# Optimization experiments

Measured on AMD Instinct MI355X. Metric: run time of the kernel, lower is better.

The kernel has to match this reference:

```python
import jax, jax.numpy as jnp
import numpy as np

NEIGHBOR_N = 3  # hard-coded in the torch module
EPS = 1e-6


def setup_inputs() -> dict:
    key = jax.random.key(0)
    k1, k2 = jax.random.split(key)
    B, P, D = 2048, 100000, 128
    sess_emb = jax.random.normal(k1, (B, D), dtype=jnp.float32)
    pool_emb = jax.random.normal(k2, (P, D), dtype=jnp.float32)
    return {"sess_emb": sess_emb, "pool_emb": pool_emb}


def reference(sess_emb, pool_emb):
    # cosine similarity: [B, P]
    fenzi = jnp.matmul(sess_emb, pool_emb.T)
    fenmu_l = jnp.sqrt(jnp.sum(sess_emb * sess_emb + EPS, axis=1))[:, None]   # [B,1]
    fenmu_r = jnp.sqrt(jnp.sum(pool_emb * pool_emb + EPS, axis=1))[None, :]   # [1,P]
    cos_sim = jax.nn.softmax(fenzi / (fenmu_l * fenmu_r), axis=-1)            # [B,P]

    k_v = min(NEIGHBOR_N, cos_sim.shape[0])
    cos_topk, topk_indice = jax.lax.top_k(cos_sim, k_v)                       # [B,k], [B,k]
    cos_topk = jax.nn.softmax(cos_topk, axis=-1)

    sess_topk = pool_emb[topk_indice]                                         # [B,k,D] gather
    neighbor_sess = jnp.sum(cos_topk[..., None] * sess_topk, axis=1)          # [B,D]
    # dropout40 is identity in eval mode; reference is deterministic
    return (neighbor_sess, cos_topk, sess_topk)
```

## Files before the change

kernel.cpp:

```cpp
#include <hip/hip_runtime.h>
#include <math.h>

#define B_ROWS 2048
#define P_ROWS 100000
#define D_DIM  128
#define NPC    64
#define NT     782
#define TILEB  32768
#define NCAND  (NPC * 3)

typedef short short8 __attribute__((ext_vector_type(8)));
typedef float f32x4  __attribute__((ext_vector_type(4)));
typedef unsigned long long u64;

__device__ __forceinline__ unsigned short f2bf(float f) {
    unsigned u = __float_as_uint(f);
    u += 0x7fffu + ((u >> 16) & 1u);
    return (unsigned short)(u >> 16);
}

__device__ __forceinline__ void async16(const char* g, char* l) {
    __builtin_amdgcn_global_load_lds(
        (const __attribute__((address_space(1))) unsigned int*)g,
        (__attribute__((address_space(3))) unsigned int*)l,
        16, 0, 0);
}

__device__ __forceinline__ void kins64(u64 k, u64& t0, u64& t1, u64& t2) {
    u64 m0 = (t0 < k) ? t0 : k;  t0 = (t0 < k) ? k : t0;
    u64 m1 = (t1 < m0) ? t1 : m0; t1 = (t1 < m0) ? m0 : t1;
    t2 = (t2 < m1) ? m1 : t2;
}

__device__ __forceinline__ void ins3d(double v, int c,
                                      double& v0, int& i0,
                                      double& v1, int& i1,
                                      double& v2, int& i2) {
    bool b0 = (v > v0) || (v == v0 && c < i0);
    bool b1 = (v > v1) || (v == v1 && c < i1);
    bool b2 = (v > v2) || (v == v2 && c < i2);
    if (b0)      { v2 = v1; i2 = i1; v1 = v0; i1 = i0; v0 = v; i0 = c; }
    else if (b1) { v2 = v1; i2 = i1; v1 = v;  i1 = c; }
    else if (b2) { v2 = v;  i2 = c; }
}

__global__ void pack_sess_kernel(const float* __restrict__ sess,
                                 char* __restrict__ sess2) {
    int row  = blockIdx.x * 4 + (threadIdx.x >> 6);
    int lane = threadIdx.x & 63;
    float2 v = ((const float2*)(sess + (size_t)row * D_DIM))[lane];
    float s = v.x * v.x + v.y * v.y;
    #pragma unroll
    for (int o = 32; o > 0; o >>= 1) s += __shfl_xor(s, o);
    float inv = 1.0f / sqrtf(s + (float)D_DIM * 1e-6f);
    ushort2 hv;
    hv.x = f2bf(v.x * inv);
    hv.y = f2bf(v.y * inv);
    *(ushort2*)(sess2 + (size_t)row * 256 + lane * 4) = hv;
}

__global__ void pack_pool_kernel(const float* __restrict__ pool,
                                 char* __restrict__ pool2,
                                 float* __restrict__ S_part) {
    __shared__ float red[128][17];
    __shared__ float s_inv[128];
    __shared__ float red2[16][128];
    const int tid = threadIdx.x;
    const int T   = blockIdx.x;
    const int c0  = tid >> 4;
    const int g   = tid & 15;

    #pragma unroll
    for (int it = 0; it < 8; ++it) {
        int c = it * 16 + c0;
        int n = T * 128 + c;
        float4 a = make_float4(0.f, 0.f, 0.f, 0.f), b = a;
        if (n < P_ROWS) {
            const float4* src = (const float4*)(pool + (size_t)n * D_DIM + g * 8);
            a = src[0]; b = src[1];
        }
        red[c][g] = a.x*a.x + a.y*a.y + a.z*a.z + a.w*a.w
                  + b.x*b.x + b.y*b.y + b.z*b.z + b.w*b.w;
    }
    __syncthreads();
    if (tid < 128) {
        float s = 0.f;
        #pragma unroll
        for (int j = 0; j < 16; ++j) s += red[tid][j];
        s_inv[tid] = 1.0f / sqrtf(s + (float)D_DIM * 1e-6f);
    }
    __syncthreads();

    float sacc[8] = {0.f,0.f,0.f,0.f,0.f,0.f,0.f,0.f};
    #pragma unroll
    for (int it = 0; it < 8; ++it) {
        int c = it * 16 + c0;
        int n = T * 128 + c;
        float4 a = make_float4(0.f, 0.f, 0.f, 0.f), b = a;
        if (n < P_ROWS) {
            const float4* src = (const float4*)(pool + (size_t)n * D_DIM + g * 8);
            a = src[0]; b = src[1];
        }
        float inv = s_inv[c];
        const float f[8] = {a.x, a.y, a.z, a.w, b.x, b.y, b.z, b.w};
        short8 hv;
        #pragma unroll
        for (int j = 0; j < 8; ++j) {
            float w = f[j] * inv;
            hv[j] = (short)f2bf(w);
            sacc[j] += w;
        }
        *(short8*)(pool2 + (size_t)T * TILEB + c * 256 + ((g ^ (c & 7)) * 16)) = hv;
    }
    #pragma unroll
    for (int j = 0; j < 8; ++j) red2[c0][g * 8 + j] = sacc[j];
    __syncthreads();
    if (tid < 128) {
        float s = 0.f;
        #pragma unroll
        for (int k = 0; k < 16; ++k) s += red2[k][tid];
        S_part[(size_t)T * 128 + tid] = s;
    }
}

__global__ void reduce_S_kernel(const float* __restrict__ S_part,
                                float* __restrict__ S) {
    __shared__ float part[256];
    const int d = blockIdx.x;
    float s = 0.f;
    for (int T = threadIdx.x; T < NT; T += 256)
        s += S_part[(size_t)T * 128 + d];
    part[threadIdx.x] = s;
    __syncthreads();
    #pragma unroll
    for (int o = 128; o > 0; o >>= 1) {
        if (threadIdx.x < o) part[threadIdx.x] += part[threadIdx.x + o];
        __syncthreads();
    }
    if (threadIdx.x == 0) S[d] = part[0];
}

__launch_bounds__(256, 2)
__global__ void gemm_topk_kernel(const char* __restrict__ sess2,
                                 const char* __restrict__ pool2,
                                 u64* __restrict__ partials) {
    __shared__ char lds[TILEB];

    const int tid = threadIdx.x;
    const int w   = tid >> 6;
    const int L   = tid & 63;
    const int q   = L >> 4;
    const int l15 = L & 15;
    const int l7  = L & 7;
    const int pc  = blockIdx.x;
    const int mt  = blockIdx.y;
    const int rowbase = mt * 128 + w * 32;

    short8 afrag[2][4];
    #pragma unroll
    for (int i = 0; i < 2; ++i)
        #pragma unroll
        for (int ks = 0; ks < 4; ++ks)
            afrag[i][ks] = *(const short8*)(sess2 +
                (size_t)(rowbase + i * 16 + l15) * 256 + (ks * 4 + q) * 16);

    int soks[4];
    #pragma unroll
    for (int ks = 0; ks < 4; ++ks) soks[ks] = ((ks * 4 + q) ^ l7) * 16;
    const char* lbase = lds + l15 * 256;

    float key0[2][4], key1[2][4], key2[2][4];
    #pragma unroll
    for (int i = 0; i < 2; ++i)
        #pragma unroll
        for (int r = 0; r < 4; ++r)
            key0[i][r] = key1[i][r] = key2[i][r] = -1e30f;

    int tloc = 0;
    for (int T = pc; T < NT; T += NPC, ++tloc) {
        __syncthreads();
        const char* tb = pool2 + (size_t)T * TILEB;
        #pragma unroll
        for (int rr = 0; rr < 8; ++rr) {
            int idx = rr * 256 + tid;
            async16(tb + idx * 16, lds + idx * 16);
        }
        __syncthreads();

        #pragma unroll
        for (int qt = 0; qt < 4; ++qt) {
            f32x4 acc[2][2];
            #pragma unroll
            for (int i = 0; i < 2; ++i) {
                acc[i][0] = (f32x4){0.f,0.f,0.f,0.f};
                acc[i][1] = (f32x4){0.f,0.f,0.f,0.f};
            }
            #pragma unroll
            for (int ks = 0; ks < 4; ++ks) {
                const char* cb = lbase + qt * 8192 + soks[ks];
                short8 b0 = *(const short8*)(cb);
                short8 b1 = *(const short8*)(cb + 16 * 256);
                #pragma unroll
                for (int i = 0; i < 2; ++i) {
                    acc[i][0] = __builtin_amdgcn_mfma_f32_16x16x32_bf16(
                        afrag[i][ks], b0, acc[i][0], 0, 0, 0);
                    acc[i][1] = __builtin_amdgcn_mfma_f32_16x16x32_bf16(
                        afrag[i][ks], b1, acc[i][1], 0, 0, 0);
                }
            }
            #pragma unroll
            for (int j = 0; j < 2; ++j) {
                const unsigned pos = (unsigned)(tloc * 8 + qt * 2 + j);
                #pragma unroll
                for (int i = 0; i < 2; ++i)
                    #pragma unroll
                    for (int r = 0; r < 4; ++r) {
                        float v = acc[i][j][r];
                        float kf = __uint_as_float(
                            (__float_as_uint(v) & 0xFFFFFF80u) | pos);
                        float o0 = key0[i][r], o1 = key1[i][r];
                        key0[i][r] = fmaxf(o0, kf);
                        key1[i][r] = __builtin_amdgcn_fmed3f(kf, o0, key1[i][r]);
                        key2[i][r] = __builtin_amdgcn_fmed3f(kf, o1, key2[i][r]);
                    }
            }
        }
    }

    #pragma unroll
    for (int i = 0; i < 2; ++i)
        #pragma unroll
        for (int r = 0; r < 4; ++r) {
            float kk[3] = {key0[i][r], key1[i][r], key2[i][r]};
            u64 t0 = 0ull, t1 = 0ull, t2 = 0ull;
            #pragma unroll
            for (int k = 0; k < 3; ++k) {
                unsigned u   = __float_as_uint(kk[k]);
                unsigned pos = u & 127u;
                unsigned vb  = u & 0xFFFFFF80u;
                unsigned mono = (vb & 0x80000000u) ? ~vb : (vb | 0x80000000u);
                unsigned col = (unsigned)((pc + (int)(pos >> 3) * NPC) * 128
                                          + (int)(pos & 7u) * 16 + l15);
                u64 key = ((u64)mono << 32) | (u64)(131071u - col);
                kins64(key, t0, t1, t2);
            }
            #pragma unroll
            for (int m = 1; m < 16; m <<= 1) {
                u64 r0 = __shfl_xor(t0, m);
                u64 r1 = __shfl_xor(t1, m);
                u64 r2 = __shfl_xor(t2, m);
                kins64(r0, t0, t1, t2);
                kins64(r1, t0, t1, t2);
                kins64(r2, t0, t1, t2);
            }
            if (l15 == 0) {
                int row = rowbase + i * 16 + q * 4 + r;
                u64* o = partials + ((size_t)row * NPC + pc) * 3;
                o[0] = t0; o[1] = t1; o[2] = t2;
            }
        }
}

__launch_bounds__(256)
__global__ void finalize_kernel(const float* __restrict__ sess,
                                const float* __restrict__ pool,
                                const u64* __restrict__ partials,
                                const float* __restrict__ S,
                                float* __restrict__ out_neighbor,
                                float* __restrict__ out_costopk,
                                float* __restrict__ out_sesstopk) {
    __shared__ u64    keys[NCAND];
    __shared__ u64    top8[8];
    __shared__ double vv[8];
    __shared__ int    ii[8];
    __shared__ double s_na, s_dss;
    __shared__ float  s_w[3];
    __shared__ int    s_i[3];

    const int row = blockIdx.x;
    const int tid = threadIdx.x;
    const int w   = tid >> 6;
    const int L   = tid & 63;

    if (tid < NCAND) keys[tid] = partials[(size_t)row * NCAND + tid];
    if (w == 3) {
        float2 sa = ((const float2*)(sess + (size_t)row * D_DIM))[L];
        double na  = (double)sa.x * sa.x + (double)sa.y * sa.y;
        double dss = (double)sa.x * S[2 * L] + (double)sa.y * S[2 * L + 1];
        #pragma unroll
        for (int o = 32; o > 0; o >>= 1) {
            na  += __shfl_xor(na, o);
            dss += __shfl_xor(dss, o);
        }
        if (L == 0) { s_na = na + (double)D_DIM * 1e-6; s_dss = dss; }
    }
    __syncthreads();

    if (w == 0) {
        for (int k = 0; k < 8; ++k) {
            u64 a0 = keys[L], a1 = keys[L + 64], a2 = keys[L + 128];
            u64 m = a0 > a1 ? a0 : a1;
            m = m > a2 ? m : a2;
            u64 g = m;
            #pragma unroll
            for (int o = 1; o < 64; o <<= 1) {
                u64 r = __shfl_xor(g, o);
                g = (r > g) ? r : g;
            }
            if (m == g && g != 0ull) {
                if (a0 == g)      keys[L] = 0ull;
                else if (a1 == g) keys[L + 64] = 0ull;
                else              keys[L + 128] = 0ull;
            }
            if (L == 0) top8[k] = g;
        }
    }
    __syncthreads();

    {
        float2 sa = ((const float2*)(sess + (size_t)row * D_DIM))[L];
        for (int cc = 0; cc < 2; ++cc) {
            int c = 2 * w + cc;
            int idx = 131071 - (int)(top8[c] & 0x1FFFFull);
            bool ok = idx < P_ROWS;
            float2 pb = ok ? ((const float2*)(pool + (size_t)idx * D_DIM))[L]
                           : make_float2(0.f, 0.f);
            double dot = (double)sa.x * pb.x + (double)sa.y * pb.y;
            double nb  = (double)pb.x * pb.x + (double)pb.y * pb.y;
            #pragma unroll
            for (int o = 32; o > 0; o >>= 1) {
                dot += __shfl_xor(dot, o);
                nb  += __shfl_xor(nb, o);
            }
            if (L == 0) {
                vv[c] = ok ? dot / sqrt(s_na * (nb + (double)D_DIM * 1e-6))
                           : -1e300;
                ii[c] = idx;
            }
        }
    }
    __syncthreads();

    if (tid == 0) {
        double v0 = -1e300, v1 = -1e300, v2 = -1e300;
        int    i0 = 0x7fffffff, i1 = 0x7fffffff, i2 = 0x7fffffff;
        for (int j = 0; j < 8; ++j) ins3d(vv[j], ii[j], v0, i0, v1, i1, v2, i2);
        double z  = (double)P_ROWS + s_dss / sqrt(s_na) + 390.625;
        double c0 = exp(v0) / z, c1 = exp(v1) / z, c2 = exp(v2) / z;
        double e1 = exp(c1 - c0), e2 = exp(c2 - c0);
        double inv = 1.0 / (1.0 + e1 + e2);
        s_w[0] = (float)inv;
        s_w[1] = (float)(e1 * inv);
        s_w[2] = (float)(e2 * inv);
        s_i[0] = i0; s_i[1] = i1; s_i[2] = i2;
    }
    __syncthreads();

    if (tid < D_DIM) {
        float g0 = pool[(size_t)s_i[0] * D_DIM + tid];
        float g1 = pool[(size_t)s_i[1] * D_DIM + tid];
        float g2 = pool[(size_t)s_i[2] * D_DIM + tid];
        out_sesstopk[((size_t)row * 3 + 0) * D_DIM + tid] = g0;
        out_sesstopk[((size_t)row * 3 + 1) * D_DIM + tid] = g1;
        out_sesstopk[((size_t)row * 3 + 2) * D_DIM + tid] = g2;
        out_neighbor[(size_t)row * D_DIM + tid] =
            s_w[0] * g0 + s_w[1] * g1 + s_w[2] * g2;
        if (tid < 3) out_costopk[row * 3 + tid] = s_w[tid];
    }
}

extern "C" void kernel_launch(void* const* d_in, const int* in_sizes, int n_in,
                              void* d_out, int out_size, void* d_ws, size_t ws_size,
                              hipStream_t stream) {
    const float* sess = (const float*)d_in[0];
    const float* pool = (const float*)d_in[1];
    float* out = (float*)d_out;
    float* out_neighbor = out;
    float* out_costopk  = out + (size_t)B_ROWS * D_DIM;
    float* out_sesstopk = out_costopk + (size_t)B_ROWS * 3;

    float* Svec     = (float*)d_ws;
    float* S_part   = (float*)((char*)d_ws + 512);
    u64*   partials = (u64*)((char*)d_ws + 512 + (size_t)NT * 128 * 4);
    char*  sess2    = (char*)partials + (size_t)B_ROWS * NCAND * 8;
    char*  pool2    = sess2 + (size_t)B_ROWS * 256;

    pack_sess_kernel<<<B_ROWS / 4, 256, 0, stream>>>(sess, sess2);
    pack_pool_kernel<<<NT, 256, 0, stream>>>(pool, pool2, S_part);
    reduce_S_kernel<<<128, 256, 0, stream>>>(S_part, Svec);

    dim3 g3(NPC, B_ROWS / 128);
    gemm_topk_kernel<<<g3, 256, 0, stream>>>(sess2, pool2, partials);

    finalize_kernel<<<B_ROWS, 256, 0, stream>>>(
        sess, pool, partials, Svec, out_neighbor, out_costopk, out_sesstopk);
}
```

Baseline: 201.9 us.

## Merge pack kernels and fold S reduction into gemm grid

Combines the session and pool packing kernels into one launch. The pool norm is now computed with wave shuffles instead of an LDS reduction, so each row is read once rather than twice. The column-sum reduction moves into an extra row of gemm_topk blocks, which cuts the pipeline from five launches to three. The cost is that some gemm blocks do unrelated reduction work, and there are fewer barriers between stages.

```diff
diff --git a/kernel.cpp b/kernel.cpp
--- a/kernel.cpp
+++ b/kernel.cpp
@@ -44,32 +44,35 @@
     else if (b2) { v2 = v;  i2 = c; }
 }
 
-__global__ void pack_sess_kernel(const float* __restrict__ sess,
-                                 char* __restrict__ sess2) {
-    int row  = blockIdx.x * 4 + (threadIdx.x >> 6);
-    int lane = threadIdx.x & 63;
-    float2 v = ((const float2*)(sess + (size_t)row * D_DIM))[lane];
-    float s = v.x * v.x + v.y * v.y;
-    #pragma unroll
-    for (int o = 32; o > 0; o >>= 1) s += __shfl_xor(s, o);
-    float inv = 1.0f / sqrtf(s + (float)D_DIM * 1e-6f);
-    ushort2 hv;
-    hv.x = f2bf(v.x * inv);
-    hv.y = f2bf(v.y * inv);
-    *(ushort2*)(sess2 + (size_t)row * 256 + lane * 4) = hv;
-}
-
-__global__ void pack_pool_kernel(const float* __restrict__ pool,
-                                 char* __restrict__ pool2,
-                                 float* __restrict__ S_part) {
-    __shared__ float red[128][17];
-    __shared__ float s_inv[128];
+__global__ void pack_kernel(const float* __restrict__ sess,
+                            const float* __restrict__ pool,
+                            char* __restrict__ sess2,
+                            char* __restrict__ pool2,
+                            float* __restrict__ S_part) {
+    const int tid = threadIdx.x;
+    const int bx  = blockIdx.x;
+
+    if (bx >= NT) {
+        int row  = (bx - NT) * 4 + (tid >> 6);
+        int lane = tid & 63;
+        float2 v = ((const float2*)(sess + (size_t)row * D_DIM))[lane];
+        float s = v.x * v.x + v.y * v.y;
+        #pragma unroll
+        for (int o = 32; o > 0; o >>= 1) s += __shfl_xor(s, o);
+        float inv = 1.0f / sqrtf(s + (float)D_DIM * 1e-6f);
+        ushort2 hv;
+        hv.x = f2bf(v.x * inv);
+        hv.y = f2bf(v.y * inv);
+        *(ushort2*)(sess2 + (size_t)row * 256 + lane * 4) = hv;
+        return;
+    }
+
     __shared__ float red2[16][128];
-    const int tid = threadIdx.x;
-    const int T   = blockIdx.x;
-    const int c0  = tid >> 4;
-    const int g   = tid & 15;
-
+    const int T  = bx;
+    const int c0 = tid >> 4;
+    const int g  = tid & 15;
+
+    float sacc[8] = {0.f,0.f,0.f,0.f,0.f,0.f,0.f,0.f};
     #pragma unroll
     for (int it = 0; it < 8; ++it) {
         int c = it * 16 + c0;
@@ -79,29 +82,13 @@
             const float4* src = (const float4*)(pool + (size_t)n * D_DIM + g * 8);
             a = src[0]; b = src[1];
         }
-        red[c][g] = a.x*a.x + a.y*a.y + a.z*a.z + a.w*a.w
-                  + b.x*b.x + b.y*b.y + b.z*b.z + b.w*b.w;
-    }
-    __syncthreads();
-    if (tid < 128) {
-        float s = 0.f;
-        #pragma unroll
-        for (int j = 0; j < 16; ++j) s += red[tid][j];
-        s_inv[tid] = 1.0f / sqrtf(s + (float)D_DIM * 1e-6f);
-    }
-    __syncthreads();
-
-    float sacc[8] = {0.f,0.f,0.f,0.f,0.f,0.f,0.f,0.f};
-    #pragma unroll
-    for (int it = 0; it < 8; ++it) {
-        int c = it * 16 + c0;
-        int n = T * 128 + c;
-        float4 a = make_float4(0.f, 0.f, 0.f, 0.f), b = a;
-        if (n < P_ROWS) {
-            const float4* src = (const float4*)(pool + (size_t)n * D_DIM + g * 8);
-            a = src[0]; b = src[1];
-        }
-        float inv = s_inv[c];
+        float s = a.x*a.x + a.y*a.y + a.z*a.z + a.w*a.w
+                + b.x*b.x + b.y*b.y + b.z*b.z + b.w*b.w;
+        s += __shfl_xor(s, 1);
+        s += __shfl_xor(s, 2);
+        s += __shfl_xor(s, 4);
+        s += __shfl_xor(s, 8);
+        float inv = 1.0f / sqrtf(s + (float)D_DIM * 1e-6f);
         const float f[8] = {a.x, a.y, a.z, a.w, b.x, b.y, b.z, b.w};
         short8 hv;
         #pragma unroll
@@ -123,37 +110,43 @@
     }
 }
 
-__global__ void reduce_S_kernel(const float* __restrict__ S_part,
-                                float* __restrict__ S) {
-    __shared__ float part[256];
-    const int d = blockIdx.x;
-    float s = 0.f;
-    for (int T = threadIdx.x; T < NT; T += 256)
-        s += S_part[(size_t)T * 128 + d];
-    part[threadIdx.x] = s;
-    __syncthreads();
-    #pragma unroll
-    for (int o = 128; o > 0; o >>= 1) {
-        if (threadIdx.x < o) part[threadIdx.x] += part[threadIdx.x + o];
-        __syncthreads();
-    }
-    if (threadIdx.x == 0) S[d] = part[0];
-}
-
 __launch_bounds__(256, 2)
 __global__ void gemm_topk_kernel(const char* __restrict__ sess2,
                                  const char* __restrict__ pool2,
-                                 u64* __restrict__ partials) {
+                                 u64* __restrict__ partials,
+                                 const float* __restrict__ S_part,
+                                 float* __restrict__ S) {
     __shared__ char lds[TILEB];
 
     const int tid = threadIdx.x;
+    const int pc  = blockIdx.x;
+    const int mt  = blockIdx.y;
+
+    if (mt == 16) {
+        float* part = (float*)lds;
+        #pragma unroll
+        for (int d2 = 0; d2 < 2; ++d2) {
+            int d = pc * 2 + d2;
+            float s = 0.f;
+            for (int T = tid; T < NT; T += 256)
+                s += S_part[(size_t)T * 128 + d];
+            part[tid] = s;
+            __syncthreads();
+            for (int o = 128; o > 0; o >>= 1) {
+                if (tid < o) part[tid] += part[tid + o];
+                __syncthreads();
+            }
+            if (tid == 0) S[d] = part[0];
+            __syncthreads();
+        }
+        return;
+    }
+
     const int w   = tid >> 6;
     const int L   = tid & 63;
     const int q   = L >> 4;
     const int l15 = L & 15;
     const int l7  = L & 7;
-    const int pc  = blockIdx.x;
-    const int mt  = blockIdx.y;
     const int rowbase = mt * 128 + w * 32;
 
     short8 afrag[2][4];
@@ -385,12 +378,10 @@
     char*  sess2    = (char*)partials + (size_t)B_ROWS * NCAND * 8;
     char*  pool2    = sess2 + (size_t)B_ROWS * 256;
 
-    pack_sess_kernel<<<B_ROWS / 4, 256, 0, stream>>>(sess, sess2);
-    pack_pool_kernel<<<NT, 256, 0, stream>>>(pool, pool2, S_part);
-    reduce_S_kernel<<<128, 256, 0, stream>>>(S_part, Svec);
-
-    dim3 g3(NPC, B_ROWS / 128);
-    gemm_topk_kernel<<<g3, 256, 0, stream>>>(sess2, pool2, partials);
+    pack_kernel<<<NT + 512, 256, 0, stream>>>(sess, pool, sess2, pool2, S_part);
+
+    dim3 g3(NPC, 17);
+    gemm_topk_kernel<<<g3, 256, 0, stream>>>(sess2, pool2, partials, S_part, Svec);
 
     finalize_kernel<<<B_ROWS, 256, 0, stream>>>(
         sess, pool, partials, Svec, out_neighbor, out_costopk, out_sesstopk);
```

After: 194.9 us. 1.04x faster.
